# Kernel optimization log

Hardware: AMD Instinct MI355X
Metric: run time of the kernel (lower is better)

The kernel has to match this reference:

```python
import jax, jax.numpy as jnp
import numpy as np

HIDDEN = 2048
N_HEADS = 32
N_KV_HEADS = 8
HEAD_DIM = 64
MAX_SEQ_LEN = 4096
ROPE_THETA = 500000.0
B, L = 1, 2048
EPS = 1e-6
NEG = -1e9


def precompute_rope(head_dim, max_seq_len, theta):
    freqs = 1.0 / theta ** (jnp.arange(0, head_dim, 2, dtype=jnp.float32) / head_dim)
    pos = jnp.arange(max_seq_len, dtype=jnp.float32)
    ang = pos[:, None] * freqs[None, :]                     # [S, hd/2]
    cos = jnp.repeat(jnp.cos(ang), 2, axis=-1)              # [S, hd]
    sin = jnp.repeat(jnp.sin(ang), 2, axis=-1)
    return cos, sin


def apply_rope(x, cos, sin):
    # x: [B, H, L, hd]; interleaved (even/odd) rotation, faithful to torch code
    seq_len = x.shape[2]
    c = cos[:seq_len][None, None, :, ::2]                   # [1,1,L,hd/2]
    s = sin[:seq_len][None, None, :, ::2]
    x1 = x[..., ::2]
    x2 = x[..., 1::2]
    o1 = x1 * c - x2 * s
    o2 = x2 * c + x1 * s
    return jnp.stack([o1, o2], axis=-1).reshape(x.shape)


def rmsnorm(x, w):
    return x * jax.lax.rsqrt(jnp.mean(x * x, axis=-1, keepdims=True) + EPS) * w


def setup_inputs() -> dict:
    key = jax.random.key(0)
    ks = jax.random.split(key, 6)
    x = jax.random.normal(ks[0], (B, L, HIDDEN), dtype=jnp.float32)
    causal = jnp.tril(jnp.ones((L, L), dtype=bool))
    mask = jnp.where(causal, 0.0, NEG).astype(jnp.float32)  # additive causal mask
    scale = 0.02
    norm_w = jnp.ones((HIDDEN,), dtype=jnp.float32)
    Wq = jax.random.normal(ks[1], (N_HEADS * HEAD_DIM, HIDDEN), dtype=jnp.float32) * scale
    Wk = jax.random.normal(ks[2], (N_KV_HEADS * HEAD_DIM, HIDDEN), dtype=jnp.float32) * scale
    Wv = jax.random.normal(ks[3], (N_KV_HEADS * HEAD_DIM, HIDDEN), dtype=jnp.float32) * scale
    Wo = jax.random.normal(ks[4], (HIDDEN, N_HEADS * HEAD_DIM), dtype=jnp.float32) * scale
    rope_cos, rope_sin = precompute_rope(HEAD_DIM, MAX_SEQ_LEN, ROPE_THETA)
    return {"x": x, "mask": mask, "norm_w": norm_w, "Wq": Wq, "Wk": Wk,
            "Wv": Wv, "Wo": Wo, "rope_cos": rope_cos, "rope_sin": rope_sin}


def reference(x, mask, norm_w, Wq, Wk, Wv, Wo, rope_cos, rope_sin):
    Bb, Ll, _ = x.shape
    residual = x
    h = rmsnorm(x, norm_w)
    q = (h @ Wq.T).reshape(Bb, Ll, N_HEADS, HEAD_DIM).transpose(0, 2, 1, 3)     # [B,H,L,hd]
    k = (h @ Wk.T).reshape(Bb, Ll, N_KV_HEADS, HEAD_DIM).transpose(0, 2, 1, 3)  # [B,Hk,L,hd]
    v = (h @ Wv.T).reshape(Bb, Ll, N_KV_HEADS, HEAD_DIM).transpose(0, 2, 1, 3)
    q = apply_rope(q, rope_cos, rope_sin)
    k = apply_rope(k, rope_cos, rope_sin)
    n_groups = N_HEADS // N_KV_HEADS
    if n_groups > 1:
        k = jnp.repeat(k, n_groups, axis=1)   # GQA repeat_interleave
        v = jnp.repeat(v, n_groups, axis=1)
    scale = jnp.sqrt(jnp.asarray(HEAD_DIM, dtype=q.dtype))
    attn = jnp.einsum('bhld,bhmd->bhlm', q, k) / scale
    attn = attn + mask                                       # broadcast [L,L]
    attn = jax.nn.softmax(attn, axis=-1)
    out = jnp.einsum('bhlm,bhmd->bhld', attn, v)
    out = out.transpose(0, 2, 1, 3).reshape(Bb, Ll, N_HEADS * HEAD_DIM)
    return out @ Wo.T + residual
```

## Files before the change

kernel.cpp:

```cpp
#include <hip/hip_runtime.h>
#include <stdint.h>

#define L_SEQ 2048
#define HID   2048
#define NHEAD 32
#define NKV   8
#define HD    64
#define KVDIM 512

typedef __attribute__((ext_vector_type(8))) short s16x8;
typedef __attribute__((ext_vector_type(4))) short s16x4;
typedef __attribute__((ext_vector_type(4))) float f32x4;

__device__ __forceinline__ short f2bf(float f) {
  __bf16 b = (__bf16)f;
  short s;
  __builtin_memcpy(&s, &b, 2);
  return s;
}

__device__ __forceinline__ void gload16(const void* g, void* l) {
  __builtin_amdgcn_global_load_lds(
      (const __attribute__((address_space(1))) void*)g,
      (__attribute__((address_space(3))) void*)l, 16, 0, 0);
}

__global__ __launch_bounds__(256) void convert_weights_kernel(
    const float* __restrict__ wq, const float* __restrict__ wk,
    const float* __restrict__ wv, const float* __restrict__ wo,
    short* __restrict__ owq, short* __restrict__ owk,
    short* __restrict__ owv, short* __restrict__ owo) {
  int64_t e = ((int64_t)blockIdx.x * 256 + threadIdx.x) * 4;
  const float* src; short* dst; int64_t o;
  if (e < 4194304)      { src = wq; dst = owq; o = e; }
  else if (e < 5242880) { src = wk; dst = owk; o = e - 4194304; }
  else if (e < 6291456) { src = wv; dst = owv; o = e - 5242880; }
  else                  { src = wo; dst = owo; o = e - 6291456; }
  f32x4 v = *(const f32x4*)(src + o);
  s16x4 b;
  b[0] = f2bf(v[0]); b[1] = f2bf(v[1]); b[2] = f2bf(v[2]); b[3] = f2bf(v[3]);
  *(s16x4*)(dst + o) = b;
}

__global__ __launch_bounds__(256) void rmsnorm_kernel(
    const float* __restrict__ x, const float* __restrict__ w,
    short* __restrict__ h) {
  const int row = blockIdx.x, tid = threadIdx.x;
  const float* xr = x + (int64_t)row * HID + tid * 8;
  f32x4 a = *(const f32x4*)(xr);
  f32x4 b = *(const f32x4*)(xr + 4);
  float ss = a[0]*a[0]+a[1]*a[1]+a[2]*a[2]+a[3]*a[3]
           + b[0]*b[0]+b[1]*b[1]+b[2]*b[2]+b[3]*b[3];
  #pragma unroll
  for (int off = 1; off < 64; off <<= 1) ss += __shfl_xor(ss, off, 64);
  __shared__ float sred[4];
  if ((tid & 63) == 0) sred[tid >> 6] = ss;
  __syncthreads();
  const float scale = rsqrtf((sred[0]+sred[1]+sred[2]+sred[3]) * (1.0f/HID) + 1e-6f);
  const float* wp = w + tid * 8;
  f32x4 wa = *(const f32x4*)(wp);
  f32x4 wb = *(const f32x4*)(wp + 4);
  s16x8 o;
  o[0]=f2bf(a[0]*scale*wa[0]); o[1]=f2bf(a[1]*scale*wa[1]);
  o[2]=f2bf(a[2]*scale*wa[2]); o[3]=f2bf(a[3]*scale*wa[3]);
  o[4]=f2bf(b[0]*scale*wb[0]); o[5]=f2bf(b[1]*scale*wb[1]);
  o[6]=f2bf(b[2]*scale*wb[2]); o[7]=f2bf(b[3]*scale*wb[3]);
  *(s16x8*)(h + (int64_t)row * HID + tid * 8) = o;
}

__device__ __forceinline__ void gemm_core_128(
    const short* __restrict__ A, const short* __restrict__ B,
    short* sA, short* sB, f32x4 acc[4][4]) {
  const int tid = threadIdx.x;
  const int lane = tid & 63;
  const int w = tid >> 6, wr = w >> 1, wc = w & 1;
  const int g = lane >> 4, li = lane & 15;

  auto stage = [&](int k0, int buf) {
    #pragma unroll
    for (int i = 0; i < 4; ++i) {
      const int flat = i * 256 + tid;
      const int row = flat >> 3, c8 = flat & 7;
      const int sc = c8 ^ (row & 7);
      gload16(A + (int64_t)row * HID + k0 + sc * 8, sA + buf * 8192 + flat * 8);
      gload16(B + (int64_t)row * HID + k0 + sc * 8, sB + buf * 8192 + flat * 8);
    }
  };

  stage(0, 0);
  for (int k0 = 0; k0 < HID; k0 += 64) {
    const int cur = (k0 >> 6) & 1;
    __syncthreads();
    if (k0 + 64 < HID) stage(k0 + 64, cur ^ 1);
    const short* cA = sA + cur * 8192;
    const short* cB = sB + cur * 8192;
    #pragma unroll
    for (int kk = 0; kk < 2; ++kk) {
      s16x8 af[4], bfr[4];
      const int chunk = (kk << 2) | g;
      #pragma unroll
      for (int m = 0; m < 4; ++m) {
        const int row = wr * 64 + m * 16 + li;
        af[m] = *(const s16x8*)(cA + row * 64 + ((chunk ^ (li & 7)) << 3));
      }
      #pragma unroll
      for (int n = 0; n < 4; ++n) {
        const int row = wc * 64 + n * 16 + li;
        bfr[n] = *(const s16x8*)(cB + row * 64 + ((chunk ^ (li & 7)) << 3));
      }
      #pragma unroll
      for (int m = 0; m < 4; ++m)
        #pragma unroll
        for (int n = 0; n < 4; ++n)
          acc[m][n] = __builtin_amdgcn_mfma_f32_16x16x32_bf16(af[m], bfr[n], acc[m][n], 0, 0, 0);
    }
  }
}

__global__ __launch_bounds__(256) void qkv_kernel(
    const short* __restrict__ h16, const short* __restrict__ wq,
    const short* __restrict__ wk, const short* __restrict__ wv,
    short* __restrict__ qo, short* __restrict__ ko, short* __restrict__ vto,
    const float* __restrict__ rc, const float* __restrict__ rs) {
  __shared__ short sA[2 * 128 * 64];
  __shared__ short sB[2 * 128 * 64];
  const int cb = blockIdx.x, rb = blockIdx.y;
  const short* B; short* out; int colbase, mode; int64_t ldc;
  if (cb < 16)      { B = wq + (int64_t)cb * 128 * HID;        out = qo;  colbase = cb * 128;        mode = 0; ldc = HID;   }
  else if (cb < 20) { B = wk + (int64_t)(cb - 16) * 128 * HID; out = ko;  colbase = (cb - 16) * 128; mode = 0; ldc = KVDIM; }
  else              { B = wv + (int64_t)(cb - 20) * 128 * HID; out = vto; colbase = (cb - 20) * 128; mode = 1; ldc = L_SEQ; }

  f32x4 acc[4][4];
  const f32x4 z = {0.f, 0.f, 0.f, 0.f};
  #pragma unroll
  for (int m = 0; m < 4; ++m)
    #pragma unroll
    for (int n = 0; n < 4; ++n) acc[m][n] = z;

  gemm_core_128(h16 + (int64_t)rb * 128 * HID, B, sA, sB, acc);

  const int lane = threadIdx.x & 63;
  const int w = threadIdx.x >> 6, wr = w >> 1, wc = w & 1;
  const int g = lane >> 4, li = lane & 15;

  if (mode == 0) {
    #pragma unroll
    for (int m = 0; m < 4; ++m) {
      #pragma unroll
      for (int n = 0; n < 4; ++n) {
        const int col = colbase + wc * 64 + n * 16 + li;
        const int d2 = col & 62;
        #pragma unroll
        for (int r = 0; r < 4; ++r) {
          const int row = rb * 128 + wr * 64 + m * 16 + g * 4 + r;
          const float c = rc[row * 64 + d2];
          const float s = rs[row * 64 + d2];
          const float v0 = acc[m][n][r];
          const float pr = __shfl_xor(v0, 1, 64);
          const float o = (lane & 1) ? (v0 * c + pr * s) : (v0 * c - pr * s);
          out[(int64_t)row * ldc + col] = f2bf(o);
        }
      }
    }
  } else {
    #pragma unroll
    for (int m = 0; m < 4; ++m) {
      #pragma unroll
      for (int n = 0; n < 4; ++n) {
        const int col = colbase + wc * 64 + n * 16 + li;
        const int row0 = rb * 128 + wr * 64 + m * 16 + g * 4;
        s16x4 pk;
        pk[0] = f2bf(acc[m][n][0]); pk[1] = f2bf(acc[m][n][1]);
        pk[2] = f2bf(acc[m][n][2]); pk[3] = f2bf(acc[m][n][3]);
        *(s16x4*)(out + (int64_t)col * L_SEQ + row0) = pk;
      }
    }
  }
}

#define CSM 0.18033688f
#define DEFER_THR 44.3614f

__device__ __forceinline__ void softmax_pv(
    f32x4 s[4], const s16x8 vf[2][4], bool diag,
    int w, int g, int li, short* sPw,
    float& m, float& l, f32x4 acc[4]) {
  if (diag) {
    const int ql = w * 16 + li;
    #pragma unroll
    for (int n = 0; n < 4; ++n)
      #pragma unroll
      for (int r = 0; r < 4; ++r)
        if (n * 16 + g * 4 + r > ql) s[n][r] = -1e30f;
  }
  float mx = fmaxf(fmaxf(s[0][0], s[0][1]), fmaxf(s[0][2], s[0][3]));
  #pragma unroll
  for (int n = 1; n < 4; ++n)
    mx = fmaxf(mx, fmaxf(fmaxf(s[n][0], s[n][1]), fmaxf(s[n][2], s[n][3])));
  mx = fmaxf(mx, __shfl_xor(mx, 16, 64));
  mx = fmaxf(mx, __shfl_xor(mx, 32, 64));
  if (__any(mx > m + DEFER_THR)) {
    const float mn = fmaxf(m, mx);
    const float al = __builtin_amdgcn_exp2f((m - mn) * CSM);
    m = mn;
    l *= al;
    #pragma unroll
    for (int dt = 0; dt < 4; ++dt)
      #pragma unroll
      for (int r = 0; r < 4; ++r) acc[dt][r] *= al;
  }
  const float nmc = -m * CSM;
  float ps = 0.f;
  #pragma unroll
  for (int n = 0; n < 4; ++n) {
    s16x4 pk;
    #pragma unroll
    for (int r = 0; r < 4; ++r) {
      const float p = __builtin_amdgcn_exp2f(fmaf(s[n][r], CSM, nmc));
      pk[r] = f2bf(p);
      ps += p;
    }
    *(s16x4*)(sPw + li * 64 + (((n * 2 + (g >> 1)) ^ (li & 7)) << 3) + (g & 1) * 4) = pk;
  }
  ps += __shfl_xor(ps, 16, 64);
  ps += __shfl_xor(ps, 32, 64);
  l += ps;
  #pragma unroll
  for (int kk = 0; kk < 2; ++kk) {
    s16x8 pf = *(const s16x8*)(sPw + li * 64 + (((kk * 4 + g) ^ (li & 7)) << 3));
    __builtin_amdgcn_s_setprio(1);
    #pragma unroll
    for (int dt = 0; dt < 4; ++dt)
      acc[dt] = __builtin_amdgcn_mfma_f32_16x16x32_bf16(vf[kk][dt], pf, acc[dt], 0, 0, 0);
    __builtin_amdgcn_s_setprio(0);
  }
}

__device__ __forceinline__ void write_out(
    const f32x4 acc[4], float l, int qb, int h, int w, int g, int li, int lane,
    short* sPw, short* __restrict__ out16) {
  const float rl = 1.0f / l;
  #pragma unroll
  for (int n2 = 0; n2 < 4; ++n2) {
    s16x4 o;
    #pragma unroll
    for (int r = 0; r < 4; ++r) o[r] = f2bf(acc[n2][r] * rl);
    *(s16x4*)(sPw + li * 64 + (((n2 * 2 + (g >> 1)) ^ (li & 7)) << 3) + (g & 1) * 4) = o;
  }
  #pragma unroll
  for (int half = 0; half < 2; ++half) {
    const int chunk = half * 64 + lane;
    const int q = chunk >> 3, c = chunk & 7;
    s16x8 v = *(const s16x8*)(sPw + q * 64 + ((c ^ (q & 7)) << 3));
    *(s16x8*)(out16 + (int64_t)(qb * 64 + w * 16 + q) * HID + h * 64 + c * 8) = v;
  }
}

__global__ __launch_bounds__(256) void attn_kernel(
    const short* __restrict__ q16, const short* __restrict__ k16,
    const short* __restrict__ vt16, short* __restrict__ out16) {
  __shared__ short sK[2 * 64 * 64];
  __shared__ short sV[2 * 64 * 64];
  __shared__ short sP[4][16 * 64];
  const int pi = blockIdx.x, h = blockIdx.y, kvh = h >> 2;
  const int qbL = pi, qbH = 31 - pi;
  const int tid = threadIdx.x, lane = tid & 63, w = tid >> 6;
  const int g = lane >> 4, li = lane & 15;
  short* sPw = &sP[w][0];

  s16x8 qfL[2], qfH[2];
  {
    const int qrL = qbL * 64 + w * 16 + li;
    const int qrH = qbH * 64 + w * 16 + li;
    #pragma unroll
    for (int kk = 0; kk < 2; ++kk) {
      qfL[kk] = *(const s16x8*)(q16 + (int64_t)qrL * HID + h * 64 + kk * 32 + g * 8);
      qfH[kk] = *(const s16x8*)(q16 + (int64_t)qrH * HID + h * 64 + kk * 32 + g * 8);
    }
  }

  f32x4 accL[4], accH[4];
  const f32x4 z = {0.f, 0.f, 0.f, 0.f};
  #pragma unroll
  for (int n = 0; n < 4; ++n) { accL[n] = z; accH[n] = z; }
  float mL = -1e30f, lL = 0.f, mH = -1e30f, lH = 0.f;

  auto stage = [&](int t, int buf) {
    const int kv0 = t * 64;
    #pragma unroll
    for (int i = 0; i < 2; ++i) {
      const int flat = i * 256 + tid;
      const int row = flat >> 3, c8 = flat & 7;
      const int sc = c8 ^ (row & 7);
      gload16(k16 + (int64_t)(kv0 + row) * KVDIM + kvh * 64 + sc * 8,
              sK + buf * 4096 + flat * 8);
      gload16(vt16 + (int64_t)(kvh * 64 + row) * L_SEQ + kv0 + sc * 8,
              sV + buf * 4096 + flat * 8);
    }
  };

  stage(0, 0);
  for (int t = 0; t <= qbH; ++t) {
    const int cur = t & 1;
    __syncthreads();
    if (t < qbH) stage(t + 1, cur ^ 1);
    const short* cK = sK + cur * 4096;
    const short* cV = sV + cur * 4096;

    s16x8 kf[2][4];
    #pragma unroll
    for (int kk = 0; kk < 2; ++kk)
      #pragma unroll
      for (int n = 0; n < 4; ++n)
        kf[kk][n] = *(const s16x8*)(cK + (n * 16 + li) * 64 + ((((kk << 2) | g) ^ (li & 7)) << 3));

    const bool doLo = (t <= qbL);
    f32x4 sH[4], sL[4];
    #pragma unroll
    for (int n = 0; n < 4; ++n) sH[n] = z;
    __builtin_amdgcn_s_setprio(1);
    #pragma unroll
    for (int kk = 0; kk < 2; ++kk)
      #pragma unroll
      for (int n = 0; n < 4; ++n)
        sH[n] = __builtin_amdgcn_mfma_f32_16x16x32_bf16(kf[kk][n], qfH[kk], sH[n], 0, 0, 0);
    __builtin_amdgcn_s_setprio(0);
    if (doLo) {
      #pragma unroll
      for (int n = 0; n < 4; ++n) sL[n] = z;
      __builtin_amdgcn_s_setprio(1);
      #pragma unroll
      for (int kk = 0; kk < 2; ++kk)
        #pragma unroll
        for (int n = 0; n < 4; ++n)
          sL[n] = __builtin_amdgcn_mfma_f32_16x16x32_bf16(kf[kk][n], qfL[kk], sL[n], 0, 0, 0);
      __builtin_amdgcn_s_setprio(0);
    }

    s16x8 vf[2][4];
    #pragma unroll
    for (int kk = 0; kk < 2; ++kk)
      #pragma unroll
      for (int dt = 0; dt < 4; ++dt)
        vf[kk][dt] = *(const s16x8*)(cV + (dt * 16 + li) * 64 + ((((kk << 2) | g) ^ (li & 7)) << 3));

    softmax_pv(sH, vf, t == qbH, w, g, li, sPw, mH, lH, accH);
    if (doLo) softmax_pv(sL, vf, t == qbL, w, g, li, sPw, mL, lL, accL);
  }

  write_out(accL, lL, qbL, h, w, g, li, lane, sPw, out16);
  write_out(accH, lH, qbH, h, w, g, li, lane, sPw, out16);
}

__global__ __launch_bounds__(256) void oproj_kernel(
    const short* __restrict__ ao, const short* __restrict__ wo,
    const float* __restrict__ resid, float* __restrict__ out) {
  __shared__ short sA[2 * 128 * 64];
  __shared__ short sB[2 * 128 * 64];
  const int cb = blockIdx.x, rb = blockIdx.y;
  f32x4 acc[4][4];
  const f32x4 z = {0.f, 0.f, 0.f, 0.f};
  #pragma unroll
  for (int m = 0; m < 4; ++m)
    #pragma unroll
    for (int n = 0; n < 4; ++n) acc[m][n] = z;

  gemm_core_128(ao + (int64_t)rb * 128 * HID, wo + (int64_t)cb * 128 * HID, sA, sB, acc);

  const int lane = threadIdx.x & 63;
  const int w = threadIdx.x >> 6, wr = w >> 1, wc = w & 1;
  const int g = lane >> 4, li = lane & 15;
  #pragma unroll
  for (int m = 0; m < 4; ++m) {
    #pragma unroll
    for (int n = 0; n < 4; ++n) {
      const int col = cb * 128 + wc * 64 + n * 16 + li;
      #pragma unroll
      for (int r = 0; r < 4; ++r) {
        const int row = rb * 128 + wr * 64 + m * 16 + g * 4 + r;
        out[(int64_t)row * HID + col] = acc[m][n][r] + resid[(int64_t)row * HID + col];
      }
    }
  }
}

extern "C" void kernel_launch(void* const* d_in, const int* in_sizes, int n_in,
                              void* d_out, int out_size, void* d_ws, size_t ws_size,
                              hipStream_t stream) {
  (void)in_sizes; (void)n_in; (void)out_size; (void)ws_size;
  const float* x      = (const float*)d_in[0];
  const float* norm_w = (const float*)d_in[2];
  const float* Wq     = (const float*)d_in[3];
  const float* Wk     = (const float*)d_in[4];
  const float* Wv     = (const float*)d_in[5];
  const float* Wo     = (const float*)d_in[6];
  const float* rc     = (const float*)d_in[7];
  const float* rs     = (const float*)d_in[8];
  float* out = (float*)d_out;

  char* ws = (char*)d_ws;
  short* wq16 = (short*)(ws);
  short* wk16 = (short*)(ws + 8388608);
  short* wv16 = (short*)(ws + 10485760);
  short* wo16 = (short*)(ws + 12582912);
  short* h16  = (short*)(ws + 20971520);
  short* q16  = (short*)(ws + 29360128);
  short* k16  = (short*)(ws + 37748736);
  short* vt16 = (short*)(ws + 39845888);
  short* ao16 = (short*)(ws + 41943040);

  convert_weights_kernel<<<10240, 256, 0, stream>>>(Wq, Wk, Wv, Wo, wq16, wk16, wv16, wo16);
  rmsnorm_kernel<<<L_SEQ, 256, 0, stream>>>(x, norm_w, h16);
  qkv_kernel<<<dim3(24, 16), 256, 0, stream>>>(h16, wq16, wk16, wv16, q16, k16, vt16, rc, rs);
  attn_kernel<<<dim3(16, NHEAD), 256, 0, stream>>>(q16, k16, vt16, ao16);
  oproj_kernel<<<dim3(16, 16), 256, 0, stream>>>(ao16, wo16, x, out);
}
```

Before: 143.5 us.

## Triple-buffer attention K/V loads, fold softmax scale into Q, merge prep kernels

The attention K/V staging moves from double to triple buffering. Explicit vmcnt waits and a raw s_barrier replace __syncthreads, so loads run two tiles ahead. The 1/sqrt(d)*log2e scale is folded into the Q RoPE epilogue, which removes an FMA per score, and the lazy rescale threshold is adjusted to match. The weight conversion and rmsnorm kernels are merged into one launch to save a launch gap, at the cost of more LDS per attention block and possible occupancy effects.

```diff
diff --git a/kernel.cpp b/kernel.cpp
--- a/kernel.cpp
+++ b/kernel.cpp
@@ -7,6 +7,7 @@
 #define NKV   8
 #define HD    64
 #define KVDIM 512
+#define QSCALE 0.18033688f
 
 typedef __attribute__((ext_vector_type(8))) short s16x8;
 typedef __attribute__((ext_vector_type(4))) short s16x4;
@@ -25,27 +26,28 @@
       (__attribute__((address_space(3))) void*)l, 16, 0, 0);
 }
 
-__global__ __launch_bounds__(256) void convert_weights_kernel(
+__global__ __launch_bounds__(256) void pre_kernel(
+    const float* __restrict__ x, const float* __restrict__ w,
     const float* __restrict__ wq, const float* __restrict__ wk,
     const float* __restrict__ wv, const float* __restrict__ wo,
+    short* __restrict__ h,
     short* __restrict__ owq, short* __restrict__ owk,
     short* __restrict__ owv, short* __restrict__ owo) {
-  int64_t e = ((int64_t)blockIdx.x * 256 + threadIdx.x) * 4;
-  const float* src; short* dst; int64_t o;
-  if (e < 4194304)      { src = wq; dst = owq; o = e; }
-  else if (e < 5242880) { src = wk; dst = owk; o = e - 4194304; }
-  else if (e < 6291456) { src = wv; dst = owv; o = e - 5242880; }
-  else                  { src = wo; dst = owo; o = e - 6291456; }
-  f32x4 v = *(const f32x4*)(src + o);
-  s16x4 b;
-  b[0] = f2bf(v[0]); b[1] = f2bf(v[1]); b[2] = f2bf(v[2]); b[3] = f2bf(v[3]);
-  *(s16x4*)(dst + o) = b;
-}
-
-__global__ __launch_bounds__(256) void rmsnorm_kernel(
-    const float* __restrict__ x, const float* __restrict__ w,
-    short* __restrict__ h) {
-  const int row = blockIdx.x, tid = threadIdx.x;
+  const int tid = threadIdx.x;
+  if (blockIdx.x >= 2048) {
+    int64_t e = ((int64_t)(blockIdx.x - 2048) * 256 + tid) * 4;
+    const float* src; short* dst; int64_t o;
+    if (e < 4194304)      { src = wq; dst = owq; o = e; }
+    else if (e < 5242880) { src = wk; dst = owk; o = e - 4194304; }
+    else if (e < 6291456) { src = wv; dst = owv; o = e - 5242880; }
+    else                  { src = wo; dst = owo; o = e - 6291456; }
+    f32x4 v = *(const f32x4*)(src + o);
+    s16x4 b;
+    b[0] = f2bf(v[0]); b[1] = f2bf(v[1]); b[2] = f2bf(v[2]); b[3] = f2bf(v[3]);
+    *(s16x4*)(dst + o) = b;
+    return;
+  }
+  const int row = blockIdx.x;
   const float* xr = x + (int64_t)row * HID + tid * 8;
   f32x4 a = *(const f32x4*)(xr);
   f32x4 b = *(const f32x4*)(xr + 4);
@@ -129,6 +131,7 @@
   if (cb < 16)      { B = wq + (int64_t)cb * 128 * HID;        out = qo;  colbase = cb * 128;        mode = 0; ldc = HID;   }
   else if (cb < 20) { B = wk + (int64_t)(cb - 16) * 128 * HID; out = ko;  colbase = (cb - 16) * 128; mode = 0; ldc = KVDIM; }
   else              { B = wv + (int64_t)(cb - 20) * 128 * HID; out = vto; colbase = (cb - 20) * 128; mode = 1; ldc = L_SEQ; }
+  const float rsc = (cb < 16) ? QSCALE : 1.0f;
 
   f32x4 acc[4][4];
   const f32x4 z = {0.f, 0.f, 0.f, 0.f};
@@ -153,8 +156,8 @@
         #pragma unroll
         for (int r = 0; r < 4; ++r) {
           const int row = rb * 128 + wr * 64 + m * 16 + g * 4 + r;
-          const float c = rc[row * 64 + d2];
-          const float s = rs[row * 64 + d2];
+          const float c = rc[row * 64 + d2] * rsc;
+          const float s = rs[row * 64 + d2] * rsc;
           const float v0 = acc[m][n][r];
           const float pr = __shfl_xor(v0, 1, 64);
           const float o = (lane & 1) ? (v0 * c + pr * s) : (v0 * c - pr * s);
@@ -178,9 +181,6 @@
   }
 }
 
-#define CSM 0.18033688f
-#define DEFER_THR 44.3614f
-
 __device__ __forceinline__ void softmax_pv(
     f32x4 s[4], const s16x8 vf[2][4], bool diag,
     int w, int g, int li, short* sPw,
@@ -199,9 +199,9 @@
     mx = fmaxf(mx, fmaxf(fmaxf(s[n][0], s[n][1]), fmaxf(s[n][2], s[n][3])));
   mx = fmaxf(mx, __shfl_xor(mx, 16, 64));
   mx = fmaxf(mx, __shfl_xor(mx, 32, 64));
-  if (__any(mx > m + DEFER_THR)) {
+  if (__any(mx > m + 8.0f)) {
     const float mn = fmaxf(m, mx);
-    const float al = __builtin_amdgcn_exp2f((m - mn) * CSM);
+    const float al = __builtin_amdgcn_exp2f(m - mn);
     m = mn;
     l *= al;
     #pragma unroll
@@ -209,14 +209,13 @@
       #pragma unroll
       for (int r = 0; r < 4; ++r) acc[dt][r] *= al;
   }
-  const float nmc = -m * CSM;
   float ps = 0.f;
   #pragma unroll
   for (int n = 0; n < 4; ++n) {
     s16x4 pk;
     #pragma unroll
     for (int r = 0; r < 4; ++r) {
-      const float p = __builtin_amdgcn_exp2f(fmaf(s[n][r], CSM, nmc));
+      const float p = __builtin_amdgcn_exp2f(s[n][r] - m);
       pk[r] = f2bf(p);
       ps += p;
     }
@@ -259,8 +258,8 @@
 __global__ __launch_bounds__(256) void attn_kernel(
     const short* __restrict__ q16, const short* __restrict__ k16,
     const short* __restrict__ vt16, short* __restrict__ out16) {
-  __shared__ short sK[2 * 64 * 64];
-  __shared__ short sV[2 * 64 * 64];
+  __shared__ short sK[3 * 64 * 64];
+  __shared__ short sV[3 * 64 * 64];
   __shared__ short sP[4][16 * 64];
   const int pi = blockIdx.x, h = blockIdx.y, kvh = h >> 2;
   const int qbL = pi, qbH = 31 - pi;
@@ -300,10 +299,15 @@
   };
 
   stage(0, 0);
+  stage(1, 1);
+  int cur = 0;
   for (int t = 0; t <= qbH; ++t) {
-    const int cur = t & 1;
-    __syncthreads();
-    if (t < qbH) stage(t + 1, cur ^ 1);
+    if (t < qbH) asm volatile("s_waitcnt vmcnt(2)" ::: "memory");
+    else         asm volatile("s_waitcnt vmcnt(0)" ::: "memory");
+    __builtin_amdgcn_sched_barrier(0);
+    __builtin_amdgcn_s_barrier();
+    __builtin_amdgcn_sched_barrier(0);
+    if (t + 2 <= qbH) stage(t + 2, cur == 0 ? 2 : cur - 1);
     const short* cK = sK + cur * 4096;
     const short* cV = sV + cur * 4096;
 
@@ -346,6 +350,8 @@
 
     softmax_pv(sH, vf, t == qbH, w, g, li, sPw, mH, lH, accH);
     if (doLo) softmax_pv(sL, vf, t == qbL, w, g, li, sPw, mL, lL, accL);
+
+    cur = (cur == 2) ? 0 : cur + 1;
   }
 
   write_out(accL, lL, qbL, h, w, g, li, lane, sPw, out16);
@@ -409,8 +415,8 @@
   short* vt16 = (short*)(ws + 39845888);
   short* ao16 = (short*)(ws + 41943040);
 
-  convert_weights_kernel<<<10240, 256, 0, stream>>>(Wq, Wk, Wv, Wo, wq16, wk16, wv16, wo16);
-  rmsnorm_kernel<<<L_SEQ, 256, 0, stream>>>(x, norm_w, h16);
+  pre_kernel<<<12288, 256, 0, stream>>>(x, norm_w, Wq, Wk, Wv, Wo,
+                                        h16, wq16, wk16, wv16, wo16);
   qkv_kernel<<<dim3(24, 16), 256, 0, stream>>>(h16, wq16, wk16, wv16, q16, k16, vt16, rc, rs);
   attn_kernel<<<dim3(16, NHEAD), 256, 0, stream>>>(q16, k16, vt16, ao16);
   oproj_kernel<<<dim3(16, 16), 256, 0, stream>>>(ao16, wo16, x, out);
```

Measured after the change: 142.8 us. No clear change (-0.6%).
